# Optimization experiments

Hardware: AMD Instinct MI355X
Metric: run time of the kernel (lower is better)

The kernel has to match this reference:

```python
import jax, jax.numpy as jnp
import numpy as np

BN_EPS = 1e-5
NUM_SUBSET = 3


def _conv1x1(x, W, b):
    # x: [B,C,T,J], W: [O,C], b: [O] -> [B,O,T,J]
    return jnp.einsum('bctj,oc->botj', x, W) + b[:, None, None]


def _bn_eval(y, gamma, beta, mean, var):
    inv = gamma / jnp.sqrt(var + BN_EPS)
    return y * inv[:, None, None] + (beta - mean * inv)[:, None, None]


def setup_inputs() -> dict:
    key = jax.random.key(0)
    ks = jax.random.split(key, 8)
    B, Cin, T, J = 64, 64, 300, 25
    Cout, inter = 128, 32
    s = 0.05
    return {
        'x': jax.random.normal(ks[0], (B, Cin, T, J), jnp.float32),
        'PA': jax.random.normal(ks[1], (NUM_SUBSET, J, J), jnp.float32) * s,
        'Wa': jax.random.normal(ks[2], (NUM_SUBSET, inter, Cin), jnp.float32) * s,
        'ba': jnp.zeros((NUM_SUBSET, inter), jnp.float32),
        'Wb': jax.random.normal(ks[3], (NUM_SUBSET, inter, Cin), jnp.float32) * s,
        'bb': jnp.zeros((NUM_SUBSET, inter), jnp.float32),
        'Wd': jax.random.normal(ks[4], (NUM_SUBSET, Cout, Cin), jnp.float32) * s,
        'bd': jnp.zeros((NUM_SUBSET, Cout), jnp.float32),
        'Wdown': jax.random.normal(ks[5], (Cout, Cin), jnp.float32) * s,
        'bdown': jnp.zeros((Cout,), jnp.float32),
        'bn_gamma': jnp.ones((Cout,), jnp.float32),
        'bn_beta': jnp.zeros((Cout,), jnp.float32),
        'bn_mean': jnp.zeros((Cout,), jnp.float32),
        'bn_var': jnp.ones((Cout,), jnp.float32),
        'down_gamma': jnp.ones((Cout,), jnp.float32),
        'down_beta': jnp.zeros((Cout,), jnp.float32),
        'down_mean': jnp.zeros((Cout,), jnp.float32),
        'down_var': jnp.ones((Cout,), jnp.float32),
    }


def reference(x, PA, Wa, ba, Wb, bb, Wd, bd, Wdown, bdown,
              bn_gamma, bn_beta, bn_mean, bn_var,
              down_gamma, down_beta, down_mean, down_var):
    B, C, T, J = x.shape
    A = PA + jnp.eye(J, dtype=x.dtype)  # [S,J,J]
    x_flat = x.reshape(B, C * T, J)
    y = None
    for i in range(NUM_SUBSET):
        # theta/phi embeddings via 1x1 convs -> [B,inter,T,J]
        A1 = _conv1x1(x, Wa[i], ba[i])
        A2 = _conv1x1(x, Wb[i], bb[i])
        A1 = A1.transpose(0, 3, 1, 2).reshape(B, J, -1)  # [B,J,inter*T]
        A2 = A2.reshape(B, -1, J)                          # [B,inter*T,J]
        scores = jnp.matmul(A1, A2) / A1.shape[-1]         # [B,J,J]
        Aadapt = jax.nn.softmax(scores, axis=-2) + A[i]    # softmax over dim -2
        z = jnp.matmul(x_flat, Aadapt).reshape(B, C, T, J)
        z = _conv1x1(z, Wd[i], bd[i])                      # [B,Cout,T,J]
        y = z if y is None else y + z
    y = _bn_eval(y, bn_gamma, bn_beta, bn_mean, bn_var)
    res = _bn_eval(_conv1x1(x, Wdown, bdown), down_gamma, down_beta, down_mean, down_var)
    return jax.nn.relu(y + res)
```

## Files before the change

kernel.cpp:

```cpp
#include <hip/hip_runtime.h>
#include <math.h>

#define T_DIM 300
#define J_DIM 25
#define CIN 64
#define COUT 128
#define B_DIM 64

typedef __attribute__((ext_vector_type(8))) short bf16x8;
typedef __attribute__((ext_vector_type(4))) float f32x4;

__device__ __forceinline__ unsigned short f2bf(float f) {
    union { float f; unsigned u; } v; v.f = f;
    unsigned r = v.u + 0x7FFF + ((v.u >> 16) & 1);
    return (unsigned short)(r >> 16);
}

__device__ __forceinline__ unsigned pkbf(float lo, float hi) {
    return (unsigned)f2bf(lo) | ((unsigned)f2bf(hi) << 16);
}

#define SC_NSEG 10
#define SC_NCH  3

__global__ __launch_bounds__(256, 2) void scores_kernel(
    const float* __restrict__ x,
    const float* __restrict__ Wa, const float* __restrict__ ba,
    const float* __restrict__ Wb, const float* __restrict__ bb,
    float* __restrict__ part)
{
    __shared__ uint4 xsf[8][256];
    __shared__ unsigned short aT1[32][328];
    __shared__ unsigned short aT2[32][328];

    const int tid  = threadIdx.x;
    const int seg  = blockIdx.x;
    const int b    = blockIdx.y;
    const int lane = tid & 63;
    const int w    = tid >> 6;
    const int g4   = lane >> 4;
    const int c16  = lane & 15;
    const int jt1  = w >> 1, jt2 = w & 1;

    const float* xb = x + (size_t)b * (CIN * T_DIM * J_DIM);

    f32x4 gacc[3];
    #pragma unroll
    for (int i = 0; i < 3; ++i) gacc[i] = (f32x4){0.f, 0.f, 0.f, 0.f};

    for (int ch = 0; ch < SC_NCH; ++ch) {
        const int pb = seg * 750 + ch * 250;

        #pragma unroll
        for (int cg = 0; cg < 8; ++cg) {
            int p = pb + tid; if (p > 7499) p = 7499;
            const float* xc = xb + (size_t)(cg * 8) * 7500 + p;
            unsigned d[4];
            #pragma unroll
            for (int m = 0; m < 4; ++m)
                d[m] = (unsigned)f2bf(xc[(2 * m) * 7500]) |
                       ((unsigned)f2bf(xc[(2 * m + 1) * 7500]) << 16);
            xsf[cg][tid] = make_uint4(d[0], d[1], d[2], d[3]);
        }
        __syncthreads();

        #pragma unroll
        for (int i = 0; i < 3; ++i) {
            #pragma unroll
            for (int pass = 0; pass < 2; ++pass) {
                const float* W  = pass ? Wb : Wa;
                const float* bs = pass ? bb : ba;
                bf16x8 afr[2][2];
                #pragma unroll
                for (int m = 0; m < 2; ++m)
                    #pragma unroll
                    for (int s = 0; s < 2; ++s) {
                        const float* wp = W + i * 2048 + (m * 16 + c16) * 64 + s * 32 + g4 * 8;
                        float4 f0 = *(const float4*)(wp);
                        float4 f1 = *(const float4*)(wp + 4);
                        bf16x8 t;
                        t[0] = f2bf(f0.x); t[1] = f2bf(f0.y); t[2] = f2bf(f0.z); t[3] = f2bf(f0.w);
                        t[4] = f2bf(f1.x); t[5] = f2bf(f1.y); t[6] = f2bf(f1.z); t[7] = f2bf(f1.w);
                        afr[m][s] = t;
                    }
                f32x4 acc[2][4];
                #pragma unroll
                for (int m = 0; m < 2; ++m) {
                    float4 bv = *(const float4*)(bs + i * 32 + m * 16 + g4 * 4);
                    #pragma unroll
                    for (int n = 0; n < 4; ++n)
                        acc[m][n] = (f32x4){bv.x, bv.y, bv.z, bv.w};
                }
                #pragma unroll
                for (int n = 0; n < 4; ++n) {
                    const int ptile = w * 4 + n;
                    #pragma unroll
                    for (int s = 0; s < 2; ++s) {
                        bf16x8 bfr = *reinterpret_cast<const bf16x8*>(&xsf[s * 4 + g4][ptile * 16 + c16]);
                        #pragma unroll
                        for (int m = 0; m < 2; ++m)
                            acc[m][n] = __builtin_amdgcn_mfma_f32_16x16x32_bf16(
                                afr[m][s], bfr, acc[m][n], 0, 0, 0);
                    }
                }
                unsigned short (*aT)[328] = pass ? aT2 : aT1;
                #pragma unroll
                for (int n = 0; n < 4; ++n) {
                    const int pos = (w * 4 + n) * 16 + c16;
                    if (pos < 250) {
                        const int t = pos / 25, j = pos - t * 25;
                        #pragma unroll
                        for (int m = 0; m < 2; ++m) {
                            const int kbase = t * 32 + m * 16 + g4 * 4;
                            uint2 pk = make_uint2(pkbf(acc[m][n][0], acc[m][n][1]),
                                                  pkbf(acc[m][n][2], acc[m][n][3]));
                            *reinterpret_cast<uint2*>(&aT[j][kbase]) = pk;
                        }
                    }
                }
            }
            __syncthreads();

            #pragma unroll
            for (int s = 0; s < 10; ++s) {
                bf16x8 af = *reinterpret_cast<const bf16x8*>(&aT1[jt1 * 16 + c16][s * 32 + g4 * 8]);
                bf16x8 bf = *reinterpret_cast<const bf16x8*>(&aT2[jt2 * 16 + c16][s * 32 + g4 * 8]);
                gacc[i] = __builtin_amdgcn_mfma_f32_16x16x32_bf16(af, bf, gacc[i], 0, 0, 0);
            }
            __syncthreads();
        }
    }

    #pragma unroll
    for (int i = 0; i < 3; ++i) {
        const int j2 = jt2 * 16 + c16;
        #pragma unroll
        for (int r = 0; r < 4; ++r) {
            const int j1 = jt1 * 16 + g4 * 4 + r;
            if (j1 < 25 && j2 < 25)
                part[((size_t)(b * 3 + i) * SC_NSEG + seg) * 625 + j1 * 25 + j2] = gacc[i][r];
        }
    }
}

__global__ void softmax_kernel(const float* __restrict__ part,
                               const float* __restrict__ PA,
                               uint4* __restrict__ Gbg)
{
    int bi = blockIdx.x;
    int b = bi / 3, i = bi - b * 3;
    int j2 = threadIdx.x;
    if (j2 >= 32) return;
    float gval[25];
    if (j2 < 25) {
        float v[25];
        float m = -1e30f;
        #pragma unroll
        for (int j1 = 0; j1 < 25; ++j1) {
            float s = 0.0f;
            for (int seg = 0; seg < SC_NSEG; ++seg)
                s += part[((size_t)bi * SC_NSEG + seg) * 625 + j1 * 25 + j2];
            v[j1] = s * (1.0f / 9600.0f);
            m = fmaxf(m, v[j1]);
        }
        float sum = 0.0f;
        #pragma unroll
        for (int j1 = 0; j1 < 25; ++j1) { v[j1] = expf(v[j1] - m); sum += v[j1]; }
        float r = 1.0f / sum;
        #pragma unroll
        for (int j1 = 0; j1 < 25; ++j1)
            gval[j1] = v[j1] * r + PA[(i * 25 + j1) * 25 + j2] + (j1 == j2 ? 1.0f : 0.0f);
    }
    #pragma unroll
    for (int kg = 0; kg < 4; ++kg) {
        unsigned d[4];
        #pragma unroll
        for (int mm = 0; mm < 4; ++mm) {
            int ja = kg * 8 + 2 * mm, jb2 = ja + 1;
            float va = (j2 < 25 && ja < 25) ? gval[ja] : 0.0f;
            float vb = (j2 < 25 && jb2 < 25) ? gval[jb2] : 0.0f;
            d[mm] = pkbf(va, vb);
        }
        Gbg[((size_t)bi * 4 + kg) * 33 + j2] = make_uint4(d[0], d[1], d[2], d[3]);
    }
}

__global__ void prep_kernel(
    const float* __restrict__ Wd, const float* __restrict__ bd,
    const float* __restrict__ Wdown, const float* __restrict__ bdown,
    const float* __restrict__ g1, const float* __restrict__ b1,
    const float* __restrict__ m1, const float* __restrict__ v1,
    const float* __restrict__ g2, const float* __restrict__ b2,
    const float* __restrict__ m2, const float* __restrict__ v2,
    unsigned short* __restrict__ Wpb, float* __restrict__ cst)
{
    const int tid = threadIdx.x;
    for (int idx = tid; idx < COUT * 256; idx += 256) {
        int o = idx >> 8, k = idx & 255;
        int region = k >> 6;
        float val;
        if (region == 1) {
            float inv = g2[o] * rsqrtf(v2[o] + 1e-5f);
            val = Wdown[o * 64 + (k & 63)] * inv;
        } else {
            int i = (region == 0) ? 0 : region - 1;
            float inv = g1[o] * rsqrtf(v1[o] + 1e-5f);
            val = Wd[(i * COUT + o) * 64 + (k & 63)] * inv;
        }
        Wpb[idx] = f2bf(val);
    }
    if (tid < COUT) {
        int o = tid;
        float inv1 = g1[o] * rsqrtf(v1[o] + 1e-5f);
        float inv2 = g2[o] * rsqrtf(v2[o] + 1e-5f);
        cst[o] = (bd[o] + bd[COUT + o] + bd[2 * COUT + o]) * inv1
               + (b1[o] - m1[o] * inv1)
               + bdown[o] * inv2
               + (b2[o] - m2[o] * inv2);
    }
}

#define M_NCH 75

__global__ __launch_bounds__(512, 8) void main_kernel(
    const float* __restrict__ x, const uint4* __restrict__ Gbg,
    const unsigned short* __restrict__ Wpb, const float* __restrict__ cst,
    float* __restrict__ out)
{
    __shared__ uint4 zxs[16][113];
    __shared__ uint4 gb[396];

    const int tid  = threadIdx.x;
    const int b    = blockIdx.y;
    const int t0   = blockIdx.x * 4;
    const int lane = tid & 63;
    const int w    = __builtin_amdgcn_readfirstlane(tid >> 6);
    const int g4   = lane >> 4;
    const int c16  = lane & 15;

    const float* xb = x + (size_t)b * (CIN * T_DIM * J_DIM) + t0 * 25;

    #pragma unroll
    for (int it = 0; it < 4; ++it) {
        const int u = tid + it * 512;
        const int quad = u & 7, t = (u >> 3) & 3, c = u >> 5;
        const int jp0 = quad * 4;
        const int kg = 8 + (c >> 3);
        const int sl = c & 7;
        #pragma unroll
        for (int e = 0; e < 4; ++e) {
            const int jp = jp0 + e;
            if (jp < 25)
                *((unsigned short*)&zxs[kg][t * 25 + jp] + sl) = f2bf(xb[c * 7500 + t * 25 + jp]);
        }
    }
    if (tid < 396) gb[tid] = Gbg[(size_t)b * 396 + tid];

    f32x4 acc[7];
    #pragma unroll
    for (int n = 0; n < 7; ++n) acc[n] = (f32x4){0.f, 0.f, 0.f, 0.f};

    const int zt = w >> 1;
    const int mh = w & 1;

    __syncthreads();

    bf16x8 a_x[2];
    #pragma unroll
    for (int m = 0; m < 2; ++m) {
        const int cA = (mh * 2 + m) * 16 + c16;
        const unsigned short* src = (const unsigned short*)&zxs[8 + (cA >> 3)][zt * 25] + (cA & 7);
        bf16x8 t;
        #pragma unroll
        for (int e = 0; e < 8; ++e) {
            const int jp = g4 * 8 + e;
            t[e] = (jp < 25) ? (short)src[jp * 8] : (short)0;
        }
        a_x[m] = t;
    }

    auto zpass = [&](int i, int kb) {
        #pragma unroll
        for (int n = 0; n < 2; ++n) {
            bf16x8 bfr = *reinterpret_cast<const bf16x8*>(&gb[(i * 4 + g4) * 33 + n * 16 + c16]);
            #pragma unroll
            for (int m = 0; m < 2; ++m) {
                f32x4 d = __builtin_amdgcn_mfma_f32_16x16x32_bf16(
                    a_x[m], bfr, (f32x4){0.f, 0.f, 0.f, 0.f}, 0, 0, 0);
                const int j = n * 16 + c16;
                if (j < 25) {
                    const int cb = (mh * 2 + m) * 16 + g4 * 4;
                    const int kg = kb + (cb >> 3);
                    const int hf = (cb >> 2) & 1;
                    unsigned lo = pkbf(d[0], d[1]), hi = pkbf(d[2], d[3]);
                    *reinterpret_cast<uint2*>(
                        reinterpret_cast<char*>(&zxs[kg][zt * 25 + j]) + hf * 8) = make_uint2(lo, hi);
                }
            }
        }
    };

    zpass(0, 0);
    __syncthreads();

    {
        const unsigned short* wrow = Wpb + (w * 16 + c16) * 256 + g4 * 8;
        #pragma unroll
        for (int kk = 0; kk < 4; ++kk) {
            bf16x8 afr = *reinterpret_cast<const bf16x8*>(wrow + kk * 32);
            #pragma unroll
            for (int n = 0; n < 7; ++n) {
                bf16x8 bfr = *reinterpret_cast<const bf16x8*>(&zxs[kk * 4 + g4][n * 16 + c16]);
                acc[n] = __builtin_amdgcn_mfma_f32_16x16x32_bf16(afr, bfr, acc[n], 0, 0, 0);
            }
        }
    }
    __syncthreads();

    zpass(1, 0);
    zpass(2, 8);
    __syncthreads();

    {
        const unsigned short* wrow = Wpb + (w * 16 + c16) * 256 + 128 + g4 * 8;
        #pragma unroll
        for (int kk = 0; kk < 4; ++kk) {
            bf16x8 afr = *reinterpret_cast<const bf16x8*>(wrow + kk * 32);
            #pragma unroll
            for (int n = 0; n < 7; ++n) {
                bf16x8 bfr = *reinterpret_cast<const bf16x8*>(&zxs[kk * 4 + g4][n * 16 + c16]);
                acc[n] = __builtin_amdgcn_mfma_f32_16x16x32_bf16(afr, bfr, acc[n], 0, 0, 0);
            }
        }
    }

    float* ob = out + (size_t)b * (COUT * T_DIM * J_DIM) + t0 * 25;
    #pragma unroll
    for (int r = 0; r < 4; ++r) {
        const int o = w * 16 + g4 * 4 + r;
        const float cv = cst[o];
        #pragma unroll
        for (int n = 0; n < 7; ++n) {
            const int pos = n * 16 + c16;
            if (pos < 100)
                ob[(size_t)o * 7500 + pos] = fmaxf(acc[n][r] + cv, 0.0f);
        }
    }
}

extern "C" void kernel_launch(void* const* d_in, const int* in_sizes, int n_in,
                              void* d_out, int out_size, void* d_ws, size_t ws_size,
                              hipStream_t stream)
{
    const float* x     = (const float*)d_in[0];
    const float* PA    = (const float*)d_in[1];
    const float* Wa    = (const float*)d_in[2];
    const float* ba    = (const float*)d_in[3];
    const float* Wb    = (const float*)d_in[4];
    const float* bb    = (const float*)d_in[5];
    const float* Wd    = (const float*)d_in[6];
    const float* bd    = (const float*)d_in[7];
    const float* Wdown = (const float*)d_in[8];
    const float* bdown = (const float*)d_in[9];
    const float* bn_g  = (const float*)d_in[10];
    const float* bn_b  = (const float*)d_in[11];
    const float* bn_m  = (const float*)d_in[12];
    const float* bn_v  = (const float*)d_in[13];
    const float* dn_g  = (const float*)d_in[14];
    const float* dn_b  = (const float*)d_in[15];
    const float* dn_m  = (const float*)d_in[16];
    const float* dn_v  = (const float*)d_in[17];

    float* ws   = (float*)d_ws;
    float* part = ws;
    uint4* Gbg  = (uint4*)(ws + 1200000);
    float* cst  = ws + 1301376;
    unsigned short* Wpb = (unsigned short*)(ws + 1301504);

    prep_kernel<<<1, 256, 0, stream>>>(Wd, bd, Wdown, bdown,
        bn_g, bn_b, bn_m, bn_v, dn_g, dn_b, dn_m, dn_v, Wpb, cst);
    scores_kernel<<<dim3(SC_NSEG, B_DIM), 256, 0, stream>>>(x, Wa, ba, Wb, bb, part);
    softmax_kernel<<<dim3(B_DIM * 3), 64, 0, stream>>>(part, PA, Gbg);
    main_kernel<<<dim3(M_NCH, B_DIM), 512, 0, stream>>>(x, Gbg, Wpb, cst, (float*)d_out);
}
```

Measured before the change: 270.5 us.

## Halve scores-kernel chunk size for occupancy and load x fragments directly in main kernel

The scores kernel now processes 125-position chunks over six iterations instead of 250 over three. This halves its shared-memory buffers and accumulator count and raises the launch-bounds occupancy target from 2 to 4 blocks per CU. In the main kernel, each wave loads its own x A-fragments straight from global memory, converts them to bf16, and writes them into shared memory, replacing the cooperative staging pass that was followed by a shared read. The trade-off is more barriers per scores block, and global loads in the main kernel that are less coalesced than before.

```diff
diff --git a/kernel.cpp b/kernel.cpp
--- a/kernel.cpp
+++ b/kernel.cpp
@@ -21,17 +21,18 @@
 }
 
 #define SC_NSEG 10
-#define SC_NCH  3
-
-__global__ __launch_bounds__(256, 2) void scores_kernel(
+#define SC_NCH  6
+#define SC_CP   125
+
+__global__ __launch_bounds__(256, 4) void scores_kernel(
     const float* __restrict__ x,
     const float* __restrict__ Wa, const float* __restrict__ ba,
     const float* __restrict__ Wb, const float* __restrict__ bb,
     float* __restrict__ part)
 {
-    __shared__ uint4 xsf[8][256];
-    __shared__ unsigned short aT1[32][328];
-    __shared__ unsigned short aT2[32][328];
+    __shared__ uint4 xsf[8][128];
+    __shared__ unsigned short aT1[32][164];
+    __shared__ unsigned short aT2[32][164];
 
     const int tid  = threadIdx.x;
     const int seg  = blockIdx.x;
@@ -49,18 +50,20 @@
     for (int i = 0; i < 3; ++i) gacc[i] = (f32x4){0.f, 0.f, 0.f, 0.f};
 
     for (int ch = 0; ch < SC_NCH; ++ch) {
-        const int pb = seg * 750 + ch * 250;
-
-        #pragma unroll
-        for (int cg = 0; cg < 8; ++cg) {
-            int p = pb + tid; if (p > 7499) p = 7499;
+        const int pb = seg * 750 + ch * SC_CP;
+
+        #pragma unroll
+        for (int uu = 0; uu < 4; ++uu) {
+            const int u  = tid + uu * 256;
+            const int cg = u >> 7, pe = u & 127;
+            const int p  = pb + ((pe < SC_CP) ? pe : (SC_CP - 1));
             const float* xc = xb + (size_t)(cg * 8) * 7500 + p;
             unsigned d[4];
             #pragma unroll
             for (int m = 0; m < 4; ++m)
                 d[m] = (unsigned)f2bf(xc[(2 * m) * 7500]) |
                        ((unsigned)f2bf(xc[(2 * m + 1) * 7500]) << 16);
-            xsf[cg][tid] = make_uint4(d[0], d[1], d[2], d[3]);
+            xsf[cg][pe] = make_uint4(d[0], d[1], d[2], d[3]);
         }
         __syncthreads();
 
@@ -83,17 +86,17 @@
                         t[4] = f2bf(f1.x); t[5] = f2bf(f1.y); t[6] = f2bf(f1.z); t[7] = f2bf(f1.w);
                         afr[m][s] = t;
                     }
-                f32x4 acc[2][4];
+                f32x4 acc[2][2];
                 #pragma unroll
                 for (int m = 0; m < 2; ++m) {
                     float4 bv = *(const float4*)(bs + i * 32 + m * 16 + g4 * 4);
                     #pragma unroll
-                    for (int n = 0; n < 4; ++n)
+                    for (int n = 0; n < 2; ++n)
                         acc[m][n] = (f32x4){bv.x, bv.y, bv.z, bv.w};
                 }
                 #pragma unroll
-                for (int n = 0; n < 4; ++n) {
-                    const int ptile = w * 4 + n;
+                for (int n = 0; n < 2; ++n) {
+                    const int ptile = w * 2 + n;
                     #pragma unroll
                     for (int s = 0; s < 2; ++s) {
                         bf16x8 bfr = *reinterpret_cast<const bf16x8*>(&xsf[s * 4 + g4][ptile * 16 + c16]);
@@ -103,11 +106,11 @@
                                 afr[m][s], bfr, acc[m][n], 0, 0, 0);
                     }
                 }
-                unsigned short (*aT)[328] = pass ? aT2 : aT1;
+                unsigned short (*aT)[164] = pass ? aT2 : aT1;
                 #pragma unroll
-                for (int n = 0; n < 4; ++n) {
-                    const int pos = (w * 4 + n) * 16 + c16;
-                    if (pos < 250) {
+                for (int n = 0; n < 2; ++n) {
+                    const int pos = (w * 2 + n) * 16 + c16;
+                    if (pos < SC_CP) {
                         const int t = pos / 25, j = pos - t * 25;
                         #pragma unroll
                         for (int m = 0; m < 2; ++m) {
@@ -122,7 +125,7 @@
             __syncthreads();
 
             #pragma unroll
-            for (int s = 0; s < 10; ++s) {
+            for (int s = 0; s < 5; ++s) {
                 bf16x8 af = *reinterpret_cast<const bf16x8*>(&aT1[jt1 * 16 + c16][s * 32 + g4 * 8]);
                 bf16x8 bf = *reinterpret_cast<const bf16x8*>(&aT2[jt2 * 16 + c16][s * 32 + g4 * 8]);
                 gacc[i] = __builtin_amdgcn_mfma_f32_16x16x32_bf16(af, bf, gacc[i], 0, 0, 0);
@@ -240,44 +243,38 @@
 
     const float* xb = x + (size_t)b * (CIN * T_DIM * J_DIM) + t0 * 25;
 
-    #pragma unroll
-    for (int it = 0; it < 4; ++it) {
-        const int u = tid + it * 512;
-        const int quad = u & 7, t = (u >> 3) & 3, c = u >> 5;
-        const int jp0 = quad * 4;
-        const int kg = 8 + (c >> 3);
-        const int sl = c & 7;
-        #pragma unroll
-        for (int e = 0; e < 4; ++e) {
-            const int jp = jp0 + e;
-            if (jp < 25)
-                *((unsigned short*)&zxs[kg][t * 25 + jp] + sl) = f2bf(xb[c * 7500 + t * 25 + jp]);
-        }
-    }
-    if (tid < 396) gb[tid] = Gbg[(size_t)b * 396 + tid];
-
-    f32x4 acc[7];
-    #pragma unroll
-    for (int n = 0; n < 7; ++n) acc[n] = (f32x4){0.f, 0.f, 0.f, 0.f};
-
     const int zt = w >> 1;
     const int mh = w & 1;
 
-    __syncthreads();
-
     bf16x8 a_x[2];
     #pragma unroll
     for (int m = 0; m < 2; ++m) {
         const int cA = (mh * 2 + m) * 16 + c16;
-        const unsigned short* src = (const unsigned short*)&zxs[8 + (cA >> 3)][zt * 25] + (cA & 7);
+        const float* src = xb + cA * 7500 + zt * 25 + g4 * 8;
+        unsigned short us[8];
         bf16x8 t;
         #pragma unroll
         for (int e = 0; e < 8; ++e) {
             const int jp = g4 * 8 + e;
-            t[e] = (jp < 25) ? (short)src[jp * 8] : (short)0;
+            const float v = (jp < 25) ? src[e] : 0.0f;
+            us[e] = f2bf(v);
+            t[e] = (short)us[e];
         }
         a_x[m] = t;
-    }
+        unsigned short* dst = (unsigned short*)&zxs[8 + (cA >> 3)][zt * 25] + (cA & 7);
+        #pragma unroll
+        for (int e = 0; e < 8; ++e) {
+            const int jp = g4 * 8 + e;
+            if (jp < 25) dst[jp * 8] = us[e];
+        }
+    }
+    if (tid < 396) gb[tid] = Gbg[(size_t)b * 396 + tid];
+
+    f32x4 acc[7];
+    #pragma unroll
+    for (int n = 0; n < 7; ++n) acc[n] = (f32x4){0.f, 0.f, 0.f, 0.f};
+
+    __syncthreads();
 
     auto zpass = [&](int i, int kb) {
         #pragma unroll
```

After: 329.3 us. 21.8% more time.
